# Kernel optimization log

Hardware: AMD Instinct MI355X
Metric: run time of the kernel (lower is better)

## Reference

```python
import jax, jax.numpy as jnp
import numpy as np

N_ENT = 100000   # entities / graph nodes
N_REL = 500      # relations (table has 2*N_REL rows: fwd+inv)
H = 256          # hidden dim
E = 320000       # edges


def setup_inputs() -> dict:
    key = jax.random.key(0)
    ks = jax.random.split(key, 9)
    std = (2.0 / (H + H)) ** 0.5  # xavier_normal for (H,H)
    return {
        "ent_emb": jax.random.normal(ks[0], (N_ENT, H), dtype=jnp.float32),
        "rel_emb": jax.random.normal(ks[1], (2 * N_REL, H), dtype=jnp.float32),
        "w_edge": jax.random.normal(ks[2], (H, H), dtype=jnp.float32) * std,
        "w_node": jax.random.normal(ks[3], (H, H), dtype=jnp.float32) * std,
        "w_comp": jax.random.normal(ks[4], (H, H), dtype=jnp.float32) * std,
        "rel_w": jax.random.normal(ks[5], (H, H), dtype=jnp.float32) * std,
        "src": jax.random.randint(ks[6], (E,), 0, N_ENT, dtype=jnp.int32),
        "dst": jax.random.randint(ks[7], (E,), 0, N_ENT, dtype=jnp.int32),
        "rel_id": jax.random.randint(ks[8], (E,), 0, 2 * N_REL, dtype=jnp.int32),
        "node_id": jnp.arange(N_ENT, dtype=jnp.int32),
    }


def _edge_softmax(score, dst, n):
    # per-destination-node softmax over incoming edges (DGL edge_softmax)
    m = jax.ops.segment_max(score, dst, num_segments=n)
    ex = jnp.exp(score - m[dst])
    s = jax.ops.segment_sum(ex, dst, num_segments=n)
    return ex / s[dst]


def reference(ent_emb, rel_emb, w_edge, w_node, w_comp, rel_w,
              src, dst, rel_id, node_id):
    n = ent_emb.shape[0]
    h = ent_emb[node_id]          # [N, H] (node_id maps node -> entity row)
    hs = h[src]                   # [E, H] source node features
    hd = h[dst]                   # [E, H] destination node features
    e = rel_emb[rel_id]           # [E, H] edge (relation) features

    # EdgeLayer: e . h_dst -> edge_softmax -> scatter-sum(e * a) -> W -> tanh
    a_e = _edge_softmax(jnp.sum(e * hd, axis=-1), dst, n)
    edge_out = jnp.tanh(
        jax.ops.segment_sum(e * a_e[:, None], dst, num_segments=n) @ w_edge)

    # NodeLayer: h_src . h_dst -> edge_softmax -> scatter-sum(h_src * a)
    a_n = _edge_softmax(jnp.sum(hs * hd, axis=-1), dst, n)
    node_out = jnp.tanh(
        jax.ops.segment_sum(hs * a_n[:, None], dst, num_segments=n) @ w_node)

    # CompLayer (mul): comp = h_src * e ; comp . h_dst -> softmax -> scatter-sum
    comp = hs * e
    a_c = _edge_softmax(jnp.sum(comp * hd, axis=-1), dst, n)
    comp_out = jnp.tanh(
        jax.ops.segment_sum(comp * a_c[:, None], dst, num_segments=n) @ w_comp)

    out_ent = ent_emb + edge_out + node_out + comp_out
    out_rel = rel_emb @ rel_w
    return (out_ent, out_rel)
```

## Files before the change

### kernel.cpp

```cpp
#include <hip/hip_runtime.h>
#include <hip/hip_bf16.h>

#define N_ENT  100000
#define N_REL2 1000
#define H      256
#define E_EDGES 320000
#define REL_ROWS_PAD 1024
#define DEG_BINS 64

typedef unsigned short u16;
typedef short bf16x8 __attribute__((ext_vector_type(8)));
typedef float floatx4 __attribute__((ext_vector_type(4)));

__device__ __forceinline__ u16 f2bf(float f) {
    unsigned x = __float_as_uint(f);
    unsigned r = (x + 0x7fffu + ((x >> 16) & 1u)) >> 16;
    return (u16)r;
}

__device__ __forceinline__ ushort4 pack4(float4 v, float s) {
    return make_ushort4(f2bf(v.x * s), f2bf(v.y * s), f2bf(v.z * s), f2bf(v.w * s));
}

__device__ __forceinline__ float fast_tanh(float x) {
    float e = __expf(2.0f * x);
    return 1.0f - 2.0f * __builtin_amdgcn_rcpf(e + 1.0f);
}

__device__ __forceinline__ void async16(u16* lds, const u16* g) {
    __builtin_amdgcn_global_load_lds(
        (const __attribute__((address_space(1))) void*)g,
        (__attribute__((address_space(3))) void*)lds, 16, 0, 0);
}

__device__ __forceinline__ float dot4(float4 a, float4 b) {
    return (a.x * b.x + a.y * b.y) + (a.z * b.z + a.w * b.w);
}
__device__ __forceinline__ float dot4m(float4 a, float4 b, float4 h) {
    return ((a.x * b.x) * h.x + (a.y * b.y) * h.y) + ((a.z * b.z) * h.z + (a.w * b.w) * h.w);
}
__device__ __forceinline__ float4 sfme(float4 a, float sc, float pr, float4 v) {
    return make_float4(a.x * sc + pr * v.x, a.y * sc + pr * v.y,
                       a.z * sc + pr * v.z, a.w * sc + pr * v.w);
}
__device__ __forceinline__ float4 sfme2(float4 a, float sc, float pr, float4 u, float4 v) {
    return make_float4(a.x * sc + (pr * u.x) * v.x, a.y * sc + (pr * u.y) * v.y,
                       a.z * sc + (pr * u.z) * v.z, a.w * sc + (pr * u.w) * v.w);
}


__global__ void hist_kernel(const int* __restrict__ dst, int* __restrict__ counts) {
    int i = blockIdx.x * blockDim.x + threadIdx.x;
    if (i < E_EDGES) atomicAdd(&counts[dst[i]], 1);
}

__global__ void scan1_kernel(const int* __restrict__ counts, int* __restrict__ offsets,
                             int* __restrict__ bsum, int* __restrict__ dbin) {
    __shared__ int buf[1024];
    __shared__ int lh[DEG_BINS];
    int t = threadIdx.x, i = blockIdx.x * 1024 + t;
    if (t < DEG_BINS) lh[t] = 0;
    int v = (i < N_ENT) ? counts[i] : 0;
    int acc = v;
    buf[t] = acc;
    __syncthreads();
    if (i < N_ENT) {
        int b = v > DEG_BINS - 1 ? DEG_BINS - 1 : v;
        atomicAdd(&lh[b], 1);
    }
    for (int off = 1; off < 1024; off <<= 1) {
        int u = (t >= off) ? buf[t - off] : 0;
        __syncthreads();
        acc += u;
        buf[t] = acc;
        __syncthreads();
    }
    if (i < N_ENT) offsets[i] = acc - v;
    if (t == 1023) bsum[blockIdx.x] = acc;
    if (t < DEG_BINS && lh[t]) atomicAdd(&dbin[t], lh[t]);
}

__global__ void scan2_kernel(int* __restrict__ bsum, int* __restrict__ offsets,
                             const int* __restrict__ dbin, int* __restrict__ doff) {
    __shared__ int s[128];
    int t = threadIdx.x;
    s[t] = (t < 98) ? bsum[t] : 0;
    __syncthreads();
    if (t == 0) {
        int run = 0;
        for (int b = 0; b < 98; ++b) { int x = s[b]; s[b] = run; run += x; }
        offsets[N_ENT] = run;
        int r2 = 0;
        for (int b = 0; b < DEG_BINS; ++b) { int x = dbin[b]; doff[b] = r2; r2 += x; }
    }
    __syncthreads();
    if (t < 98) bsum[t] = s[t];
}

__global__ void scan3_kernel(int* __restrict__ offsets, const int* __restrict__ bsum) {
    int i = blockIdx.x * 1024 + threadIdx.x;
    if (i < N_ENT && blockIdx.x > 0) offsets[i] += bsum[blockIdx.x];
}

__global__ void degplace_kernel(const int* __restrict__ counts, int* __restrict__ doff,
                                int* __restrict__ dorder) {
    __shared__ int lh[DEG_BINS];
    __shared__ int lbase[DEG_BINS];
    int t = threadIdx.x;
    if (t < DEG_BINS) lh[t] = 0;
    __syncthreads();
    int i = blockIdx.x * blockDim.x + t;
    int b = 0, myidx = 0;
    if (i < N_ENT) {
        b = counts[i]; if (b > DEG_BINS - 1) b = DEG_BINS - 1;
        myidx = atomicAdd(&lh[b], 1);
    }
    __syncthreads();
    if (t < DEG_BINS) lbase[t] = lh[t] ? atomicAdd(&doff[t], lh[t]) : 0;
    __syncthreads();
    if (i < N_ENT) dorder[lbase[b] + myidx] = i;
}

__global__ void place_kernel(const int* __restrict__ dst, const int* __restrict__ src,
                             const int* __restrict__ rel_id, const int* __restrict__ node_id,
                             const int* __restrict__ offsets,
                             int* __restrict__ counts, int2* __restrict__ meta) {
    int i = blockIdx.x * blockDim.x + threadIdx.x;
    if (i < E_EDGES) {
        int d = dst[i];
        int old = atomicSub(&counts[d], 1);
        meta[offsets[d] + old - 1] = make_int2(node_id[src[i]], rel_id[i]);
    }
}

__global__ void swz_kernel(const float* __restrict__ w0, const float* __restrict__ w1,
                           const float* __restrict__ w2, const float* __restrict__ w3,
                           u16* __restrict__ dstp) {
    int t = blockIdx.x * blockDim.x + threadIdx.x;
    if (t >= 4 * H * H) return;
    int mat = t >> 16;
    int r = t & 65535;
    int j = r & 7, lane = (r >> 3) & 63, kstep = (r >> 9) & 7, ntile = r >> 12;
    int k = kstep * 32 + (lane >> 4) * 8 + j;
    int n = ntile * 16 + (lane & 15);
    const float* W = (mat == 0) ? w0 : (mat == 1) ? w1 : (mat == 2) ? w2 : w3;
    dstp[t] = f2bf(W[k * H + n]);
}

__global__ void relbf_kernel(const float* __restrict__ rel, u16* __restrict__ out) {
    int t = blockIdx.x * blockDim.x + threadIdx.x;
    if (t >= REL_ROWS_PAD * H) return;
    int row = t >> 8, kk = t & 255;
    int k = kk ^ ((row & 7) << 3);
    float v = (row < N_REL2) ? rel[row * H + k] : 0.f;
    out[t] = f2bf(v);
}

__global__ __launch_bounds__(256) void scatter_kernel(
    const float* __restrict__ ent, const float* __restrict__ rel,
    const int2* __restrict__ meta, const int* __restrict__ node_id,
    const int* __restrict__ offsets, const int* __restrict__ dorder,
    u16* __restrict__ agg_e, u16* __restrict__ agg_n, u16* __restrict__ agg_c) {
    int lane = threadIdx.x & 63;
    int wv = threadIdx.x >> 6;
    int grp = lane >> 4, sl = lane & 15;
    int w = blockIdx.x * 16 + wv * 4 + grp;
    int d = dorder[w];
    int nid = node_id[d];
    int p0 = offsets[d], p1 = offsets[d + 1];
    const float4* hrow = (const float4*)(ent + (size_t)nid * H);
    float4 h0 = hrow[sl], h1 = hrow[16 + sl], h2 = hrow[32 + sl], h3 = hrow[48 + sl];
    float me = -INFINITY, mn = -INFINITY, mc = -INFINITY;
    float le = 0.f, ln = 0.f, lc = 0.f;
    float4 z = make_float4(0.f, 0.f, 0.f, 0.f);
    float4 ae0 = z, ae1 = z, ae2 = z, ae3 = z;
    float4 an0 = z, an1 = z, an2 = z, an3 = z;
    float4 ac0 = z, ac1 = z, ac2 = z, ac3 = z;

    for (int pc = p0; pc < p1; ++pc) {
        int2 md = meta[pc];
        const float4* er = (const float4*)(rel + (size_t)md.y * H);
        const float4* sr = (const float4*)(ent + (size_t)md.x * H);
        float4 e0 = er[sl], e1 = er[16 + sl], e2 = er[32 + sl], e3 = er[48 + sl];
        float4 s0 = sr[sl], s1 = sr[16 + sl], s2 = sr[32 + sl], s3 = sr[48 + sl];
        float de = dot4(e0, h0) + dot4(e1, h1) + dot4(e2, h2) + dot4(e3, h3);
        float dn = dot4(s0, h0) + dot4(s1, h1) + dot4(s2, h2) + dot4(s3, h3);
        float dc = dot4m(e0, s0, h0) + dot4m(e1, s1, h1) + dot4m(e2, s2, h2) + dot4m(e3, s3, h3);
#pragma unroll
        for (int o = 8; o; o >>= 1) {
            de += __shfl_xor(de, o);
            dn += __shfl_xor(dn, o);
            dc += __shfl_xor(dc, o);
        }
        { float nm = fmaxf(me, de); float sc = __expf(me - nm); float pr = __expf(de - nm);
          le = le * sc + pr;
          ae0 = sfme(ae0, sc, pr, e0); ae1 = sfme(ae1, sc, pr, e1);
          ae2 = sfme(ae2, sc, pr, e2); ae3 = sfme(ae3, sc, pr, e3); me = nm; }
        { float nm = fmaxf(mn, dn); float sc = __expf(mn - nm); float pr = __expf(dn - nm);
          ln = ln * sc + pr;
          an0 = sfme(an0, sc, pr, s0); an1 = sfme(an1, sc, pr, s1);
          an2 = sfme(an2, sc, pr, s2); an3 = sfme(an3, sc, pr, s3); mn = nm; }
        { float nm = fmaxf(mc, dc); float sc = __expf(mc - nm); float pr = __expf(dc - nm);
          lc = lc * sc + pr;
          ac0 = sfme2(ac0, sc, pr, e0, s0); ac1 = sfme2(ac1, sc, pr, e1, s1);
          ac2 = sfme2(ac2, sc, pr, e2, s2); ac3 = sfme2(ac3, sc, pr, e3, s3); mc = nm; }
    }
    float ie  = (le > 0.f) ? 1.0f / le : 0.f;
    float in_ = (ln > 0.f) ? 1.0f / ln : 0.f;
    float ic  = (lc > 0.f) ? 1.0f / lc : 0.f;
    size_t rowb = (size_t)d * 512;
    int swz = (d & 7) << 4;
    int b0 = sl * 8;
    *(ushort4*)((char*)agg_e + rowb + ((b0      ) ^ swz)) = pack4(ae0, ie);
    *(ushort4*)((char*)agg_e + rowb + ((b0 + 128) ^ swz)) = pack4(ae1, ie);
    *(ushort4*)((char*)agg_e + rowb + ((b0 + 256) ^ swz)) = pack4(ae2, ie);
    *(ushort4*)((char*)agg_e + rowb + ((b0 + 384) ^ swz)) = pack4(ae3, ie);
    *(ushort4*)((char*)agg_n + rowb + ((b0      ) ^ swz)) = pack4(an0, in_);
    *(ushort4*)((char*)agg_n + rowb + ((b0 + 128) ^ swz)) = pack4(an1, in_);
    *(ushort4*)((char*)agg_n + rowb + ((b0 + 256) ^ swz)) = pack4(an2, in_);
    *(ushort4*)((char*)agg_n + rowb + ((b0 + 384) ^ swz)) = pack4(an3, in_);
    *(ushort4*)((char*)agg_c + rowb + ((b0      ) ^ swz)) = pack4(ac0, ic);
    *(ushort4*)((char*)agg_c + rowb + ((b0 + 128) ^ swz)) = pack4(ac1, ic);
    *(ushort4*)((char*)agg_c + rowb + ((b0 + 256) ^ swz)) = pack4(ac2, ic);
    *(ushort4*)((char*)agg_c + rowb + ((b0 + 384) ^ swz)) = pack4(ac3, ic);
}

__global__ __launch_bounds__(256, 2) void gemm_kernel(
    const u16* __restrict__ A0, const u16* __restrict__ A1, const u16* __restrict__ A2,
    const u16* __restrict__ W0, const u16* __restrict__ W1, const u16* __restrict__ W2,
    const float* __restrict__ base, float* __restrict__ out,
    int n_real, int n_layers, int do_tanh) {
    __shared__ u16 lA[2][16384];
    int tid = threadIdx.x;
    int lane = tid & 63;
    int wv = tid >> 6;
    int m = lane & 15;
    int quad = lane >> 4;
    int r0 = blockIdx.x * 64;
    const u16* As[3] = { A0, A1, A2 };
    const u16* Ws[3] = { W0, W1, W2 };

    float outacc[4][4][4];
#pragma unroll
    for (int rt = 0; rt < 4; ++rt)
#pragma unroll
        for (int ct = 0; ct < 4; ++ct) {
            int grow = r0 + rt * 16 + quad * 4;
            int gcol = wv * 64 + ct * 16 + m;
#pragma unroll
            for (int r = 0; r < 4; ++r) {
                float v = 0.f;
                if (base != nullptr && (grow + r) < n_real) v = base[(size_t)(grow + r) * H + gcol];
                outacc[rt][ct][r] = v;
            }
        }

    {
        const u16* gsrc = As[0] + (size_t)blockIdx.x * 64 * H;
#pragma unroll
        for (int rnd = 0; rnd < 8; ++rnd) {
            int off8 = (rnd * 256 + tid) * 8;
            async16(&lA[0][off8], gsrc + off8);
        }
    }

    int mrow = m * 512;
    int swz = (m & 7) << 4;

    for (int l = 0; l < n_layers; ++l) {
        __syncthreads();
        if (l + 1 < n_layers) {
            const u16* gsrc = As[l + 1] + (size_t)blockIdx.x * 64 * H;
            u16* dstb = lA[(l + 1) & 1];
#pragma unroll
            for (int rnd = 0; rnd < 8; ++rnd) {
                int off8 = (rnd * 256 + tid) * 8;
                async16(&dstb[off8], gsrc + off8);
            }
        }
        const char* lbc = (const char*)lA[l & 1];
        const u16* Wl = Ws[l];

        floatx4 lacc[4][4];
#pragma unroll
        for (int rt = 0; rt < 4; ++rt)
#pragma unroll
            for (int ct = 0; ct < 4; ++ct)
#pragma unroll
                for (int r = 0; r < 4; ++r) lacc[rt][ct][r] = 0.f;

#pragma unroll
        for (int ks = 0; ks < 8; ++ks) {
            bf16x8 af[4], bfr[4];
#pragma unroll
            for (int rt = 0; rt < 4; ++rt)
                af[rt] = *(const bf16x8*)(lbc + rt * 8192 + mrow + ((ks * 64 + quad * 16) ^ swz));
#pragma unroll
            for (int ct = 0; ct < 4; ++ct)
                bfr[ct] = *(const bf16x8*)(Wl + (((size_t)(wv * 4 + ct) * 8 + ks) * 64 + lane) * 8);
#pragma unroll
            for (int rt = 0; rt < 4; ++rt)
#pragma unroll
                for (int ct = 0; ct < 4; ++ct)
                    lacc[rt][ct] = __builtin_amdgcn_mfma_f32_16x16x32_bf16(
                        af[rt], bfr[ct], lacc[rt][ct], 0, 0, 0);
        }

#pragma unroll
        for (int rt = 0; rt < 4; ++rt)
#pragma unroll
            for (int ct = 0; ct < 4; ++ct)
#pragma unroll
                for (int r = 0; r < 4; ++r) {
                    float v = lacc[rt][ct][r];
                    outacc[rt][ct][r] += do_tanh ? fast_tanh(v) : v;
                }
    }

#pragma unroll
    for (int rt = 0; rt < 4; ++rt)
#pragma unroll
        for (int ct = 0; ct < 4; ++ct) {
            int grow = r0 + rt * 16 + quad * 4;
            int gcol = wv * 64 + ct * 16 + m;
#pragma unroll
            for (int r = 0; r < 4; ++r)
                if ((grow + r) < n_real) out[(size_t)(grow + r) * H + gcol] = outacc[rt][ct][r];
        }
}


extern "C" void kernel_launch(void* const* d_in, const int* in_sizes, int n_in,
                              void* d_out, int out_size, void* d_ws, size_t ws_size,
                              hipStream_t stream) {
    (void)in_sizes; (void)n_in; (void)out_size; (void)ws_size;
    const float* ent    = (const float*)d_in[0];
    const float* rel    = (const float*)d_in[1];
    const float* w_edge = (const float*)d_in[2];
    const float* w_node = (const float*)d_in[3];
    const float* w_comp = (const float*)d_in[4];
    const float* rel_w  = (const float*)d_in[5];
    const int* src      = (const int*)d_in[6];
    const int* dst      = (const int*)d_in[7];
    const int* rel_id   = (const int*)d_in[8];
    const int* node_id  = (const int*)d_in[9];

    char* wsb = (char*)d_ws;
    size_t o = 0;
    auto alloc = [&](size_t bytes) -> char* {
        char* p = wsb + o;
        o = (o + bytes + 255) & ~(size_t)255;
        return p;
    };
    int* counts  = (int*)alloc((size_t)N_ENT * 4);
    int* offsets = (int*)alloc((size_t)(N_ENT + 1) * 4);
    int* bsum    = (int*)alloc(128 * 4);
    int2* meta   = (int2*)alloc((size_t)E_EDGES * 8);
    int* dbin    = (int*)alloc(DEG_BINS * 4);
    int* doff    = (int*)alloc(DEG_BINS * 4);
    int* dorder  = (int*)alloc((size_t)N_ENT * 4);
    u16* agg_e   = (u16*)alloc((size_t)N_ENT * H * 2);
    u16* agg_n   = (u16*)alloc((size_t)N_ENT * H * 2);
    u16* agg_c   = (u16*)alloc((size_t)N_ENT * H * 2);
    u16* wswz    = (u16*)alloc((size_t)4 * H * H * 2);
    u16* relbf   = (u16*)alloc((size_t)REL_ROWS_PAD * H * 2);
    (void)alloc(65536);

    float* out_ent = (float*)d_out;
    float* out_rel = out_ent + (size_t)N_ENT * H;

    hipMemsetAsync(counts, 0, (size_t)N_ENT * 4, stream);
    hipMemsetAsync(dbin, 0, DEG_BINS * 4, stream);
    hist_kernel<<<(E_EDGES + 255) / 256, 256, 0, stream>>>(dst, counts);
    scan1_kernel<<<98, 1024, 0, stream>>>(counts, offsets, bsum, dbin);
    scan2_kernel<<<1, 128, 0, stream>>>(bsum, offsets, dbin, doff);
    scan3_kernel<<<98, 1024, 0, stream>>>(offsets, bsum);
    degplace_kernel<<<98, 1024, 0, stream>>>(counts, doff, dorder);
    place_kernel<<<(E_EDGES + 255) / 256, 256, 0, stream>>>(dst, src, rel_id, node_id,
                                                            offsets, counts, meta);
    swz_kernel<<<(4 * H * H + 255) / 256, 256, 0, stream>>>(w_edge, w_node, w_comp, rel_w, wswz);
    relbf_kernel<<<(REL_ROWS_PAD * H + 255) / 256, 256, 0, stream>>>(rel, relbf);
    scatter_kernel<<<N_ENT / 16, 256, 0, stream>>>(ent, rel, meta, node_id, offsets, dorder,
                                                   agg_e, agg_n, agg_c);
    gemm_kernel<<<(N_ENT + 63) / 64, 256, 0, stream>>>(agg_e, agg_n, agg_c,
                                                       wswz, wswz + H * H, wswz + 2 * H * H,
                                                       ent, out_ent, N_ENT, 3, 1);
    gemm_kernel<<<(N_REL2 + 63) / 64, 256, 0, stream>>>(relbf, relbf, relbf,
                                                        wswz + 3 * H * H, wswz + 3 * H * H, wswz + 3 * H * H,
                                                        nullptr, out_rel, N_REL2, 1, 0);
}
```

Baseline: 474.1 us.

## Load GEMM A fragments directly from global memory, dropping LDS staging and swizzle

The GEMM kernel no longer stages each 64-row A tile into double-buffered LDS with async global-to-LDS loads. Each wave now reads its bf16x8 A fragments straight from global memory, and the XOR swizzle is removed from the scatter writes and the relation bf16 conversion to match. With the 64 KB of shared memory gone, launch bounds rise to 4 blocks per CU to raise occupancy. The cost is that all four waves re-read the same A rows from global memory or L2 instead of sharing them in LDS, and the load latency is no longer overlapped by the prefetch.

```diff
diff --git a/kernel.cpp b/kernel.cpp
--- a/kernel.cpp
+++ b/kernel.cpp
@@ -25,12 +25,6 @@
 __device__ __forceinline__ float fast_tanh(float x) {
     float e = __expf(2.0f * x);
     return 1.0f - 2.0f * __builtin_amdgcn_rcpf(e + 1.0f);
-}
-
-__device__ __forceinline__ void async16(u16* lds, const u16* g) {
-    __builtin_amdgcn_global_load_lds(
-        (const __attribute__((address_space(1))) void*)g,
-        (__attribute__((address_space(3))) void*)lds, 16, 0, 0);
 }
 
 __device__ __forceinline__ float dot4(float4 a, float4 b) {
@@ -150,8 +144,7 @@
 __global__ void relbf_kernel(const float* __restrict__ rel, u16* __restrict__ out) {
     int t = blockIdx.x * blockDim.x + threadIdx.x;
     if (t >= REL_ROWS_PAD * H) return;
-    int row = t >> 8, kk = t & 255;
-    int k = kk ^ ((row & 7) << 3);
+    int row = t >> 8, k = t & 255;
     float v = (row < N_REL2) ? rel[row * H + k] : 0.f;
     out[t] = f2bf(v);
 }
@@ -209,28 +202,26 @@
     float in_ = (ln > 0.f) ? 1.0f / ln : 0.f;
     float ic  = (lc > 0.f) ? 1.0f / lc : 0.f;
     size_t rowb = (size_t)d * 512;
-    int swz = (d & 7) << 4;
     int b0 = sl * 8;
-    *(ushort4*)((char*)agg_e + rowb + ((b0      ) ^ swz)) = pack4(ae0, ie);
-    *(ushort4*)((char*)agg_e + rowb + ((b0 + 128) ^ swz)) = pack4(ae1, ie);
-    *(ushort4*)((char*)agg_e + rowb + ((b0 + 256) ^ swz)) = pack4(ae2, ie);
-    *(ushort4*)((char*)agg_e + rowb + ((b0 + 384) ^ swz)) = pack4(ae3, ie);
-    *(ushort4*)((char*)agg_n + rowb + ((b0      ) ^ swz)) = pack4(an0, in_);
-    *(ushort4*)((char*)agg_n + rowb + ((b0 + 128) ^ swz)) = pack4(an1, in_);
-    *(ushort4*)((char*)agg_n + rowb + ((b0 + 256) ^ swz)) = pack4(an2, in_);
-    *(ushort4*)((char*)agg_n + rowb + ((b0 + 384) ^ swz)) = pack4(an3, in_);
-    *(ushort4*)((char*)agg_c + rowb + ((b0      ) ^ swz)) = pack4(ac0, ic);
-    *(ushort4*)((char*)agg_c + rowb + ((b0 + 128) ^ swz)) = pack4(ac1, ic);
-    *(ushort4*)((char*)agg_c + rowb + ((b0 + 256) ^ swz)) = pack4(ac2, ic);
-    *(ushort4*)((char*)agg_c + rowb + ((b0 + 384) ^ swz)) = pack4(ac3, ic);
-}
-
-__global__ __launch_bounds__(256, 2) void gemm_kernel(
+    *(ushort4*)((char*)agg_e + rowb + b0      ) = pack4(ae0, ie);
+    *(ushort4*)((char*)agg_e + rowb + b0 + 128) = pack4(ae1, ie);
+    *(ushort4*)((char*)agg_e + rowb + b0 + 256) = pack4(ae2, ie);
+    *(ushort4*)((char*)agg_e + rowb + b0 + 384) = pack4(ae3, ie);
+    *(ushort4*)((char*)agg_n + rowb + b0      ) = pack4(an0, in_);
+    *(ushort4*)((char*)agg_n + rowb + b0 + 128) = pack4(an1, in_);
+    *(ushort4*)((char*)agg_n + rowb + b0 + 256) = pack4(an2, in_);
+    *(ushort4*)((char*)agg_n + rowb + b0 + 384) = pack4(an3, in_);
+    *(ushort4*)((char*)agg_c + rowb + b0      ) = pack4(ac0, ic);
+    *(ushort4*)((char*)agg_c + rowb + b0 + 128) = pack4(ac1, ic);
+    *(ushort4*)((char*)agg_c + rowb + b0 + 256) = pack4(ac2, ic);
+    *(ushort4*)((char*)agg_c + rowb + b0 + 384) = pack4(ac3, ic);
+}
+
+__global__ __launch_bounds__(256, 4) void gemm_kernel(
     const u16* __restrict__ A0, const u16* __restrict__ A1, const u16* __restrict__ A2,
     const u16* __restrict__ W0, const u16* __restrict__ W1, const u16* __restrict__ W2,
     const float* __restrict__ base, float* __restrict__ out,
     int n_real, int n_layers, int do_tanh) {
-    __shared__ u16 lA[2][16384];
     int tid = threadIdx.x;
     int lane = tid & 63;
     int wv = tid >> 6;
@@ -255,30 +246,8 @@
             }
         }
 
-    {
-        const u16* gsrc = As[0] + (size_t)blockIdx.x * 64 * H;
-#pragma unroll
-        for (int rnd = 0; rnd < 8; ++rnd) {
-            int off8 = (rnd * 256 + tid) * 8;
-            async16(&lA[0][off8], gsrc + off8);
-        }
-    }
-
-    int mrow = m * 512;
-    int swz = (m & 7) << 4;
-
     for (int l = 0; l < n_layers; ++l) {
-        __syncthreads();
-        if (l + 1 < n_layers) {
-            const u16* gsrc = As[l + 1] + (size_t)blockIdx.x * 64 * H;
-            u16* dstb = lA[(l + 1) & 1];
-#pragma unroll
-            for (int rnd = 0; rnd < 8; ++rnd) {
-                int off8 = (rnd * 256 + tid) * 8;
-                async16(&dstb[off8], gsrc + off8);
-            }
-        }
-        const char* lbc = (const char*)lA[l & 1];
+        const char* Al = (const char*)(As[l]) + (size_t)r0 * 512;
         const u16* Wl = Ws[l];
 
         floatx4 lacc[4][4];
@@ -294,7 +263,7 @@
             bf16x8 af[4], bfr[4];
 #pragma unroll
             for (int rt = 0; rt < 4; ++rt)
-                af[rt] = *(const bf16x8*)(lbc + rt * 8192 + mrow + ((ks * 64 + quad * 16) ^ swz));
+                af[rt] = *(const bf16x8*)(Al + (size_t)(rt * 16 + m) * 512 + ks * 64 + quad * 16);
 #pragma unroll
             for (int ct = 0; ct < 4; ++ct)
                 bfr[ct] = *(const bf16x8*)(Wl + (((size_t)(wv * 4 + ct) * 8 + ks) * 64 + lane) * 8);
```

Measured after the change: 695.7 us. +46.8%, slower.
